# Kernel tuning notes

Measured on AMD Instinct MI355X. Metric: run time of the kernel, lower is better.

## Reference

```python
import jax, jax.numpy as jnp
import numpy as np

B = 512       # batch
N = 64        # max_nodes
H = 256       # hidden_dim
LAT = 128     # latent_dim
HEADS = 4
HC = H // HEADS   # per-head channels (GATConv out_channels)
NF = 64       # node_features
L = 3         # num_dec_layers
R = 8         # lora_r
SCAL = 16.0 / R   # lora_alpha / r
NB = 4        # num_bond_types
SLOPE = 0.2   # GATConv leaky_relu negative slope


def setup_inputs() -> dict:
    key = jax.random.key(0)
    ks = jax.random.split(key, 21)
    f = lambda k, shape, s=0.05: jax.random.normal(k, shape, dtype=jnp.float32) * s
    Din = H + LAT  # GAT input dim = hidden + latent (concat)
    return {
        "z": jax.random.normal(ks[0], (B, LAT), dtype=jnp.float32),
        # z_to_nodes LoRALinear: latent -> hidden*max_nodes
        "z2n_w": f(ks[1], (H * N, LAT)), "z2n_b": f(ks[2], (H * N,)),
        "z2n_A": f(ks[3], (R, LAT)), "z2n_B": f(ks[4], (H * N, R)),
        # GATConv stacks (same Din every layer): lin weight, att_src, att_dst, bias
        "gat_W": f(ks[5], (L, HEADS * HC, Din)),
        "gat_asrc": f(ks[6], (L, HEADS, HC)),
        "gat_adst": f(ks[7], (L, HEADS, HC)),
        "gat_bias": f(ks[8], (L, H)),
        # node predictor LoRALinear: hidden -> node_features
        "node_w": f(ks[9], (NF, H)), "node_b": f(ks[10], (NF,)),
        "node_A": f(ks[11], (R, H)), "node_B": f(ks[12], (NF, R)),
        # adj predictor LoRALinear: 2*hidden -> 1
        "adj_w": f(ks[13], (1, 2 * H)), "adj_b": f(ks[14], (1,)),
        "adj_A": f(ks[15], (R, 2 * H)), "adj_B": f(ks[16], (1, R)),
        # bond type predictor LoRALinear: 2*hidden -> 4
        "bond_w": f(ks[17], (NB, 2 * H)), "bond_b": f(ks[18], (NB,)),
        "bond_A": f(ks[19], (R, 2 * H)), "bond_B": f(ks[20], (NB, R)),
    }


def _lora_w(W, A, Bm):
    # effective weight of LoRALinear (eval mode, dropout off): W + (alpha/r) * B @ A
    return W + SCAL * (Bm @ A)


def _forward(z, z2n_w, z2n_b, z2n_A, z2n_B, gat_W, gat_asrc, gat_adst, gat_bias,
             node_w, node_b, node_A, node_B, adj_w, adj_b, adj_A, adj_B,
             bond_w, bond_b, bond_A, bond_B):
    # z_to_nodes: LoRA linear + ReLU -> [B, N, H]
    x = jax.nn.relu(z @ _lora_w(z2n_w, z2n_A, z2n_B).T + z2n_b).reshape(B, N, H)
    z_bc = jnp.broadcast_to(z[:, None, :], (B, N, LAT))
    # Fully-connected graph (off-diagonal edges) + GATConv default self loops
    # => dense softmax attention over all N source nodes per target, per graph.
    for l in range(L):
        xc = jnp.concatenate([x, z_bc], axis=-1)                      # [B,N,H+LAT]
        Wr = gat_W[l].reshape(HEADS, HC, H + LAT)
        h = jnp.einsum('bnd,hcd->bnhc', xc, Wr)                        # [B,N,heads,HC]
        e_src = jnp.einsum('bnhc,hc->bnh', h, gat_asrc[l])             # source term
        e_dst = jnp.einsum('bnhc,hc->bnh', h, gat_adst[l])             # target term
        e = e_dst[:, :, None, :] + e_src[:, None, :, :]                # [B,i,j,heads]
        e = jnp.where(e > 0, e, SLOPE * e)                             # leaky_relu
        alpha = jax.nn.softmax(e, axis=2)                              # over sources j
        out = jnp.einsum('bijh,bjhc->bihc', alpha, h).reshape(B, N, H) + gat_bias[l]
        x = jax.nn.relu(out)
    # node reconstruction
    recon_nodes = x @ _lora_w(node_w, node_A, node_B).T + node_b       # [B,N,NF]
    # pairwise predictors: Linear(concat[h_i,h_j]) = W1 h_i + W2 h_j + b
    iu = jnp.triu(jnp.ones((N, N), dtype=bool), 1)
    Wa = _lora_w(adj_w, adj_A, adj_B)                                  # [1,2H]
    s1 = x @ Wa[:, :H].T                                               # [B,N,1]
    s2 = x @ Wa[:, H:].T
    Am = s1 + jnp.swapaxes(s2, 1, 2) + adj_b[0]                        # Am[i,j]=s1[i]+s2[j]
    adj_logits = jnp.where(iu, Am, jnp.where(iu.T, jnp.swapaxes(Am, 1, 2), 0.0))
    Wb = _lora_w(bond_w, bond_A, bond_B)                               # [NB,2H]
    t1 = x @ Wb[:, :H].T                                               # [B,N,NB]
    t2 = x @ Wb[:, H:].T
    Bm = t1[:, :, None, :] + t2[:, None, :, :] + bond_b                # [B,N,N,NB]
    bond_logits = jnp.where(iu[:, :, None], Bm,
                            jnp.where(iu.T[:, :, None], jnp.swapaxes(Bm, 1, 2), 0.0))
    return recon_nodes, adj_logits, bond_logits


def reference(z, z2n_w, z2n_b, z2n_A, z2n_B, gat_W, gat_asrc, gat_adst, gat_bias,
              node_w, node_b, node_A, node_B, adj_w, adj_b, adj_A, adj_B,
              bond_w, bond_b, bond_A, bond_B):
    return _forward(z, z2n_w, z2n_b, z2n_A, z2n_B, gat_W, gat_asrc, gat_adst, gat_bias,
                    node_w, node_b, node_A, node_B, adj_w, adj_b, adj_A, adj_B,
                    bond_w, bond_b, bond_A, bond_B)
```

## Files before the change

kernel.cpp:

```cpp
#include <hip/hip_runtime.h>


typedef float float4v __attribute__((ext_vector_type(4)));
typedef short short8v __attribute__((ext_vector_type(8)));
typedef uint  uint4v  __attribute__((ext_vector_type(4)));

struct alignas(8) us4 { ushort x, y, z, w; };

#define ZA_OFF 0UL
#define HZ_OFF 4096UL
#define EZ_OFF 397312UL
#define XBF_U   819200UL
#define ZBF_U   9207808UL
#define GWBF_U  9273344UL
#define WZBF_U  9568256UL
#define PW_U    11665408UL
#define WST_U   11759616UL

__device__ inline ushort f2bf(float f) {
    uint u = __float_as_uint(f);
    uint r = (u + 0x7FFFu + ((u >> 16) & 1u)) >> 16;
    return (ushort)r;
}
__device__ inline float bf2f(ushort u) { return __uint_as_float(((uint)u) << 16); }

__device__ inline uint cvtpk(float a, float b) {
    uint r;
    asm("v_cvt_pk_bf16_f32 %0, %1, %2" : "=v"(r) : "v"(a), "v"(b));
    return r;
}

__device__ inline int xidx(int r, int cu) {
    int ch = cu >> 3;
    return r * 256 + (((ch ^ (r & 7))) << 3) + (cu & 7);
}

struct P3 { short8v b0, b1, b2; };
__device__ inline P3 loadP3(const ushort* pw, int lo, int hi, int kk) {
    P3 f;
    f.b0 = *(const short8v*)(pw + (size_t)(      lo)*256 + kk*32 + hi*8);
    f.b1 = *(const short8v*)(pw + (size_t)(16  + lo)*256 + kk*32 + hi*8);
    f.b2 = *(const short8v*)(pw + (size_t)(32  + lo)*256 + kk*32 + hi*8);
    return f;
}
struct P2 { short8v b3, b4; };
__device__ inline P2 loadP2(const ushort* pw, int lo, int hi, int kk) {
    P2 f;
    f.b3 = *(const short8v*)(pw + (size_t)(48 + lo)*256 + kk*32 + hi*8);
    f.b4 = *(const short8v*)(pw + (size_t)(64 + lo)*256 + kk*32 + hi*8);
    return f;
}

__device__ inline void gll(const ushort* src, ushort* dst) {
    __builtin_amdgcn_global_load_lds(
        (const __attribute__((address_space(1))) void*)src,
        (__attribute__((address_space(3))) void*)dst, 16, 0, 0);
}

__device__ inline void stageW(ushort* dstHead, const ushort* srcHead, int c0h, int ln) {
    if (c0h == 0) {
        gll(srcHead +        ln*8, dstHead);
        gll(srcHead +  512 + ln*8, dstHead + 512);
        gll(srcHead + 2048 + ln*8, dstHead + 2048);
    } else {
        gll(srcHead + 1024 + ln*8, dstHead + 1024);
        gll(srcHead + 1536 + ln*8, dstHead + 1536);
    }
}

__global__ __launch_bounds__(256) void k_setup(
    const float* __restrict__ z, const float* __restrict__ z2nA,
    const float* __restrict__ nodeW, const float* __restrict__ nodeA, const float* __restrict__ nodeB,
    const float* __restrict__ adjW, const float* __restrict__ adjA, const float* __restrict__ adjB,
    const float* __restrict__ bondW, const float* __restrict__ bondA, const float* __restrict__ bondB,
    const float* __restrict__ gatW, const float* __restrict__ z2nw,
    const float* __restrict__ asrcp, const float* __restrict__ adstp,
    float* __restrict__ wsf)
{
    ushort* wsu = (ushort*)wsf;
    int gid = blockIdx.x * 256 + threadIdx.x;
    if (gid < 4096) {
        int b = gid >> 3, r = gid & 7;
        const float* zp = z + (size_t)b * 128;
        const float* ap = z2nA + (size_t)r * 128;
        float s = 0.f;
        #pragma unroll 8
        for (int k = 0; k < 128; ++k) s += zp[k] * ap[k];
        wsf[ZA_OFF + gid] = s;
    } else if (gid < 24576) {
        int idx = gid - 4096;
        int r = idx >> 8, c = idx & 255;
        float v = 0.f;
        if (r < 64) {
            float s = 0.f;
            #pragma unroll
            for (int k = 0; k < 8; ++k) s += nodeB[r*8+k] * nodeA[k*256+c];
            v = nodeW[r*256+c] + 2.0f * s;
        } else if (r < 66) {
            int off = (r - 64) * 256 + c;
            float s = 0.f;
            #pragma unroll
            for (int k = 0; k < 8; ++k) s += adjB[k] * adjA[k*512+off];
            v = adjW[off] + 2.0f * s;
        } else if (r < 70) {
            int q = r - 66;
            float s = 0.f;
            #pragma unroll
            for (int k = 0; k < 8; ++k) s += bondB[q*8+k] * bondA[k*512+c];
            v = bondW[q*512+c] + 2.0f * s;
        } else if (r < 74) {
            int q = r - 70;
            float s = 0.f;
            #pragma unroll
            for (int k = 0; k < 8; ++k) s += bondB[q*8+k] * bondA[k*512+256+c];
            v = bondW[q*512+256+c] + 2.0f * s;
        }
        wsu[PW_U + idx] = f2bf(v);
    } else if (gid < 55296) {
        int idx = gid - 24576;
        int lkk = idx / 1280;
        int rem = idx - lkk * 1280;
        int head = rem / 320;
        int rem2 = rem - head * 320;
        int frag = rem2 >> 6;
        int ln = rem2 & 63;
        int lo = ln & 15, hi = ln >> 4;
        int l = lkk >> 3, kk = lkk & 7;
        ushort* dst = wsu + WST_U + (size_t)idx * 8;
        if (frag < 4) {
            const float* srcw = gatW + ((size_t)(l*256 + head*64 + frag*16 + lo))*384 + kk*32 + hi*8;
            #pragma unroll
            for (int j = 0; j < 8; ++j) dst[j] = f2bf(srcw[j]);
        } else {
            float s[8] = {0.f,0.f,0.f,0.f,0.f,0.f,0.f,0.f};
            if (lo < 2) {
                const float* av = (lo == 0 ? asrcp : adstp) + l*256 + head*64;
                const float* wp = gatW + ((size_t)(l*256 + head*64))*384 + kk*32 + hi*8;
                for (int hc = 0; hc < 64; ++hc) {
                    float a = av[hc];
                    const float* wr = wp + (size_t)hc * 384;
                    #pragma unroll
                    for (int j = 0; j < 8; ++j) s[j] += wr[j] * a;
                }
            }
            #pragma unroll
            for (int j = 0; j < 8; ++j) dst[j] = f2bf(s[j]);
        }
    } else {
        int cid = gid - 55296;
        const float* src; ushort* dst; int idx;
        if (cid < 16384)        { src = z;     dst = wsu + ZBF_U;  idx = cid; }
        else if (cid < 90112)   { src = gatW;  dst = wsu + GWBF_U; idx = cid - 16384; }
        else if (cid < 614400)  { src = z2nw;  dst = wsu + WZBF_U; idx = cid - 90112; }
        else return;
        float4 v = ((const float4*)src)[idx];
        us4 o; o.x = f2bf(v.x); o.y = f2bf(v.y); o.z = f2bf(v.z); o.w = f2bf(v.w);
        ((us4*)dst)[idx] = o;
    }
}

__global__ __launch_bounds__(256) void k_z2n(
    const float* __restrict__ bias, const float* __restrict__ lB,
    const float* __restrict__ asrcp, const float* __restrict__ adstp,
    float* __restrict__ wsf)
{
    ushort* wsu = (ushort*)wsf;
    int t = threadIdx.x;
    int w = t >> 6, ln = t & 63, lo = ln & 15, hi = ln >> 4;

    if (blockIdx.x >= 512) {
        int bid2 = blockIdx.x - 512;
        int l = bid2 >> 3, bg = bid2 & 7;
        const ushort* wz = wsu + GWBF_U + (size_t)l * 98304;
        const ushort* zb = wsu + ZBF_U + (size_t)bg * 64 * 128;
        float4v acc[4][4];
        #pragma unroll
        for (int m = 0; m < 4; ++m)
            #pragma unroll
            for (int n = 0; n < 4; ++n) acc[m][n] = (float4v)(0.f);
        #pragma unroll
        for (int kk = 0; kk < 4; ++kk) {
            short8v a[4], bq[4];
            #pragma unroll
            for (int m = 0; m < 4; ++m)
                a[m] = *(const short8v*)(wz + (size_t)(w*64 + m*16 + lo)*384 + 256 + kk*32 + hi*8);
            #pragma unroll
            for (int n = 0; n < 4; ++n)
                bq[n] = *(const short8v*)(zb + (size_t)(n*16 + lo)*128 + kk*32 + hi*8);
            #pragma unroll
            for (int m = 0; m < 4; ++m)
                #pragma unroll
                for (int n = 0; n < 4; ++n)
                    acc[m][n] = __builtin_amdgcn_mfma_f32_16x16x32_bf16(a[m], bq[n], acc[m][n], 0, 0, 0);
        }
        float* hzp = wsf + HZ_OFF + (size_t)l * 131072;
        #pragma unroll
        for (int m = 0; m < 4; ++m)
            #pragma unroll
            for (int n = 0; n < 4; ++n)
                #pragma unroll
                for (int q = 0; q < 4; ++q)
                    hzp[(size_t)(bg*64 + n*16 + lo)*256 + w*64 + m*16 + hi*4 + q] = acc[m][n][q];
        float as_[4][4], ad_[4][4];
        #pragma unroll
        for (int m = 0; m < 4; ++m)
            #pragma unroll
            for (int q = 0; q < 4; ++q) {
                as_[m][q] = asrcp[l*256 + w*64 + m*16 + hi*4 + q];
                ad_[m][q] = adstp[l*256 + w*64 + m*16 + hi*4 + q];
            }
        #pragma unroll
        for (int n = 0; n < 4; ++n) {
            float ss = 0.f, dd = 0.f;
            #pragma unroll
            for (int m = 0; m < 4; ++m)
                #pragma unroll
                for (int q = 0; q < 4; ++q) {
                    ss += acc[m][n][q] * as_[m][q];
                    dd += acc[m][n][q] * ad_[m][q];
                }
            ss += __shfl_xor(ss, 16); ss += __shfl_xor(ss, 32);
            dd += __shfl_xor(dd, 16); dd += __shfl_xor(dd, 32);
            if (hi == 0) {
                int b = bg*64 + n*16 + lo;
                wsf[EZ_OFF + (size_t)(l*2 + 0)*2048 + (size_t)b*4 + w] = ss;
                wsf[EZ_OFF + (size_t)(l*2 + 1)*2048 + (size_t)b*4 + w] = dd;
            }
        }
        return;
    }

    int bm = blockIdx.x >> 6, bn = blockIdx.x & 63;
    int brow0 = bm * 64;
    int o0 = bn * 256 + w * 64;
    const ushort* wz = wsu + WZBF_U;
    const ushort* zb = wsu + ZBF_U;
    float4v acc[4][4];
    #pragma unroll
    for (int m = 0; m < 4; ++m)
        #pragma unroll
        for (int n = 0; n < 4; ++n) acc[m][n] = (float4v)(0.f);
    #pragma unroll
    for (int kk = 0; kk < 4; ++kk) {
        short8v a[4], bq[4];
        #pragma unroll
        for (int m = 0; m < 4; ++m)
            a[m] = *(const short8v*)(wz + (size_t)(o0 + m*16 + lo)*128 + kk*32 + hi*8);
        #pragma unroll
        for (int n = 0; n < 4; ++n)
            bq[n] = *(const short8v*)(zb + (size_t)(brow0 + n*16 + lo)*128 + kk*32 + hi*8);
        #pragma unroll
        for (int m = 0; m < 4; ++m)
            #pragma unroll
            for (int n = 0; n < 4; ++n)
                acc[m][n] = __builtin_amdgcn_mfma_f32_16x16x32_bf16(a[m], bq[n], acc[m][n], 0, 0, 0);
    }
    const float* zA = wsf + ZA_OFF;
    float4 za0[4], za1[4];
    #pragma unroll
    for (int n = 0; n < 4; ++n) {
        int brow = brow0 + n*16 + lo;
        za0[n] = *(const float4*)&zA[brow*8];
        za1[n] = *(const float4*)&zA[brow*8 + 4];
    }
    #pragma unroll
    for (int m = 0; m < 4; ++m) {
        float lor[4][4]; float bs[4];
        #pragma unroll
        for (int q = 0; q < 4; ++q) {
            int o = o0 + m*16 + hi*4 + q;
            float4 b20 = *(const float4*)&lB[(size_t)o*8];
            float4 b21 = *(const float4*)&lB[(size_t)o*8 + 4];
            bs[q] = bias[o];
            #pragma unroll
            for (int n = 0; n < 4; ++n)
                lor[n][q] = za0[n].x*b20.x + za0[n].y*b20.y + za0[n].z*b20.z + za0[n].w*b20.w
                          + za1[n].x*b21.x + za1[n].y*b21.y + za1[n].z*b21.z + za1[n].w*b21.w;
        }
        #pragma unroll
        for (int n = 0; n < 4; ++n) {
            int brow = brow0 + n*16 + lo;
            float v0 = acc[m][n][0] + 2.f*lor[n][0] + bs[0]; v0 = v0 > 0.f ? v0 : 0.f;
            float v1 = acc[m][n][1] + 2.f*lor[n][1] + bs[1]; v1 = v1 > 0.f ? v1 : 0.f;
            float v2 = acc[m][n][2] + 2.f*lor[n][2] + bs[2]; v2 = v2 > 0.f ? v2 : 0.f;
            float v3 = acc[m][n][3] + 2.f*lor[n][3] + bs[3]; v3 = v3 > 0.f ? v3 : 0.f;
            us4 pk; pk.x = f2bf(v0); pk.y = f2bf(v1); pk.z = f2bf(v2); pk.w = f2bf(v3);
            *(us4*)(wsu + XBF_U + (size_t)brow*16384 + o0 + m*16 + hi*4) = pk;
        }
    }
}

__global__ __launch_bounds__(512, 4) void k_fused(
    const float* __restrict__ gbias,
    const float* __restrict__ nodeb, const float* __restrict__ adjb,
    const float* __restrict__ bondb,
    float* __restrict__ wsf, float* __restrict__ out)
{
    extern __shared__ ushort dyn[];
    ushort* Rr   = dyn;
    ushort* bbuf = dyn + 17408;
    float*  scr  = (float*)(dyn + 17408 + 20480);
    ushort* wsu = (ushort*)wsf;
    int t = threadIdx.x;
    int w = t >> 6, ln = t & 63, lo = ln & 15, hi = ln >> 4;
    int head = w & 3, m0 = (w >> 2) * 32;
    int headH = w >> 1, c0h = w & 1;
    int b = blockIdx.x;
    const ushort* xb = wsu + XBF_U + (size_t)b * 16384;

    #pragma unroll
    for (int i = 0; i < 4; ++i) {
        int flat = i*512 + t;
        int r = flat >> 5, ch = flat & 31;
        short8v v = *(const short8v*)(xb + (size_t)r*256 + ch*8);
        *(short8v*)&Rr[r*256 + ((ch ^ (r & 7)) << 3)] = v;
    }
    __syncthreads();

    float* es = scr;
    float* ed = scr + 256;

    {
        const ushort* wst0 = wsu + WST_U;
        stageW(bbuf +         headH*2560, wst0 +         headH*2560, c0h, ln);
        stageW(bbuf + 10240 + headH*2560, wst0 + 10240 + headH*2560, c0h, ln);
    }

    for (int l = 0; l < 3; ++l) {
        const ushort* wst  = wsu + WST_U + (size_t)l * 81920;
        const ushort* wstN = wsu + WST_U + (size_t)(l + 1) * 81920;
        const float*  hzp = wsf + HZ_OFF + (size_t)l*131072 + (size_t)b*256 + headH*64;

        float hzA = hzp[(c0h*2    )*16 + lo];
        float hzB = hzp[(c0h*2 + 1)*16 + lo];
        float ezs = wsf[EZ_OFF + (size_t)(l*2 + 0)*2048 + (size_t)b*4 + headH];
        float ezd = wsf[EZ_OFF + (size_t)(l*2 + 1)*2048 + (size_t)b*4 + headH];

        float4v acc[2][4], accE[4];
        float eInit = (lo == 0) ? ezs : (lo == 1 ? ezd : 0.f);
        #pragma unroll
        for (int m = 0; m < 4; ++m) {
            acc[0][m] = (float4v)(hzA);
            acc[1][m] = (float4v)(hzB);
            accE[m]   = (float4v)(eInit);
        }

        #pragma unroll
        for (int kk = 0; kk < 8; ++kk) {
            if (kk == 7 && l == 2) {
                asm volatile("s_waitcnt vmcnt(0)" ::: "memory");
            } else if (c0h == 0) {
                asm volatile("s_waitcnt vmcnt(3)" ::: "memory");
            } else {
                asm volatile("s_waitcnt vmcnt(2)" ::: "memory");
            }
            const ushort* bb = bbuf + (kk&1)*10240 + headH*2560;
            short8v bq0 = *(const short8v*)(bb + (c0h*2    )*512 + ln*8);
            short8v bq1 = *(const short8v*)(bb + (c0h*2 + 1)*512 + ln*8);
            short8v bsd = {};
            if (c0h == 0) bsd = *(const short8v*)(bb + 2048 + ln*8);
            short8v a0 = *(const short8v*)&Rr[xidx(     lo, kk*32 + hi*8)];
            short8v a1 = *(const short8v*)&Rr[xidx(16 + lo, kk*32 + hi*8)];
            short8v a2 = *(const short8v*)&Rr[xidx(32 + lo, kk*32 + hi*8)];
            short8v a3 = *(const short8v*)&Rr[xidx(48 + lo, kk*32 + hi*8)];
            if (kk < 6) {
                asm volatile("s_waitcnt lgkmcnt(0)" ::: "memory");
                stageW(bbuf + (kk&1)*10240 + headH*2560,
                       wst + (size_t)(kk+2)*10240 + headH*2560, c0h, ln);
            } else if (l < 2) {
                asm volatile("s_waitcnt lgkmcnt(0)" ::: "memory");
                stageW(bbuf + (kk&1)*10240 + headH*2560,
                       wstN + (size_t)(kk-6)*10240 + headH*2560, c0h, ln);
            }
            __builtin_amdgcn_s_setprio(1);
            acc[0][0] = __builtin_amdgcn_mfma_f32_16x16x32_bf16(a0, bq0, acc[0][0], 0, 0, 0);
            acc[0][1] = __builtin_amdgcn_mfma_f32_16x16x32_bf16(a1, bq0, acc[0][1], 0, 0, 0);
            acc[0][2] = __builtin_amdgcn_mfma_f32_16x16x32_bf16(a2, bq0, acc[0][2], 0, 0, 0);
            acc[0][3] = __builtin_amdgcn_mfma_f32_16x16x32_bf16(a3, bq0, acc[0][3], 0, 0, 0);
            acc[1][0] = __builtin_amdgcn_mfma_f32_16x16x32_bf16(a0, bq1, acc[1][0], 0, 0, 0);
            acc[1][1] = __builtin_amdgcn_mfma_f32_16x16x32_bf16(a1, bq1, acc[1][1], 0, 0, 0);
            acc[1][2] = __builtin_amdgcn_mfma_f32_16x16x32_bf16(a2, bq1, acc[1][2], 0, 0, 0);
            acc[1][3] = __builtin_amdgcn_mfma_f32_16x16x32_bf16(a3, bq1, acc[1][3], 0, 0, 0);
            if (c0h == 0) {
                accE[0] = __builtin_amdgcn_mfma_f32_16x16x32_bf16(a0, bsd, accE[0], 0, 0, 0);
                accE[1] = __builtin_amdgcn_mfma_f32_16x16x32_bf16(a1, bsd, accE[1], 0, 0, 0);
                accE[2] = __builtin_amdgcn_mfma_f32_16x16x32_bf16(a2, bsd, accE[2], 0, 0, 0);
                accE[3] = __builtin_amdgcn_mfma_f32_16x16x32_bf16(a3, bsd, accE[3], 0, 0, 0);
            }
            __builtin_amdgcn_s_setprio(0);
        }

        if (c0h == 0) {
            if (lo == 0) {
                #pragma unroll
                for (int m = 0; m < 4; ++m)
                    *(float4*)&es[headH*64 + m*16 + hi*4] =
                        make_float4(accE[m][0], accE[m][1], accE[m][2], accE[m][3]);
            } else if (lo == 1) {
                #pragma unroll
                for (int m = 0; m < 4; ++m)
                    *(float4*)&ed[headH*64 + m*16 + hi*4] =
                        make_float4(accE[m][0], accE[m][1], accE[m][2], accE[m][3]);
            }
        }

        __syncthreads();

        #pragma unroll
        for (int cf = 0; cf < 2; ++cf)
            #pragma unroll
            for (int m = 0; m < 4; ++m) {
                uint2 pk;
                pk.x = cvtpk(acc[cf][m][0], acc[cf][m][1]);
                pk.y = cvtpk(acc[cf][m][2], acc[cf][m][3]);
                *(uint2*)&Rr[headH*4352 + ((c0h*2 + cf)*16 + lo)*68 + m*16 + hi*4] = pk;
            }

        __syncthreads();

        float4v acc2[4][2];
        #pragma unroll
        for (int m = 0; m < 4; ++m)
            #pragma unroll
            for (int n = 0; n < 2; ++n) acc2[m][n] = (float4v)(0.f);
        float psum[2] = {0.f, 0.f};
        #pragma unroll
        for (int kk = 0; kk < 2; ++kk) {
            short8v hb[4];
            #pragma unroll
            for (int m = 0; m < 4; ++m)
                hb[m] = *(const short8v*)&Rr[head*4352 + (m*16 + lo)*68 + kk*32 + hi*8];
            float4 e0 = *(const float4*)&es[head*64 + kk*32 + hi*8];
            float4 e1 = *(const float4*)&es[head*64 + kk*32 + hi*8 + 4];
            float ej[8] = {e0.x, e0.y, e0.z, e0.w, e1.x, e1.y, e1.z, e1.w};
            #pragma unroll
            for (int n = 0; n < 2; ++n) {
                float edr = ed[head*64 + m0 + n*16 + lo];
                float pvv[8]; float pp = 0.f;
                #pragma unroll
                for (int jj = 0; jj < 8; ++jj) {
                    float e = edr + ej[jj];
                    e = fmaxf(e, 0.2f * e);
                    float p = __expf(e);
                    pp += p;
                    pvv[jj] = p;
                }
                uint4v au;
                au.x = cvtpk(pvv[0], pvv[1]); au.y = cvtpk(pvv[2], pvv[3]);
                au.z = cvtpk(pvv[4], pvv[5]); au.w = cvtpk(pvv[6], pvv[7]);
                short8v af = __builtin_bit_cast(short8v, au);
                psum[n] += pp;
                __builtin_amdgcn_s_setprio(1);
                #pragma unroll
                for (int m = 0; m < 4; ++m)
                    acc2[m][n] = __builtin_amdgcn_mfma_f32_16x16x32_bf16(hb[m], af, acc2[m][n], 0, 0, 0);
                __builtin_amdgcn_s_setprio(0);
            }
        }
        float rs[2];
        #pragma unroll
        for (int n = 0; n < 2; ++n) {
            psum[n] += __shfl_xor(psum[n], 16);
            psum[n] += __shfl_xor(psum[n], 32);
            rs[n] = 1.0f / psum[n];
        }

        __syncthreads();

        #pragma unroll
        for (int m = 0; m < 4; ++m) {
            int c0 = head*64 + m*16 + hi*4;
            float b0f = gbias[l*256 + c0 + 0];
            float b1f = gbias[l*256 + c0 + 1];
            float b2f = gbias[l*256 + c0 + 2];
            float b3f = gbias[l*256 + c0 + 3];
            #pragma unroll
            for (int n = 0; n < 2; ++n) {
                int r = m0 + n*16 + lo;
                float v0 = acc2[m][n][0]*rs[n] + b0f; v0 = v0 > 0.f ? v0 : 0.f;
                float v1 = acc2[m][n][1]*rs[n] + b1f; v1 = v1 > 0.f ? v1 : 0.f;
                float v2 = acc2[m][n][2]*rs[n] + b2f; v2 = v2 > 0.f ? v2 : 0.f;
                float v3 = acc2[m][n][3]*rs[n] + b3f; v3 = v3 > 0.f ? v3 : 0.f;
                uint2 pk; pk.x = cvtpk(v0, v1); pk.y = cvtpk(v2, v3);
                *(uint2*)&Rr[xidx(r, c0)] = pk;
            }
        }

        __syncthreads();
    }

    const ushort* pw = wsu + PW_U;
    int pq = w & 3, pn = w >> 2;
    if (pn == 0) {
        float4v p0 = (float4v)(0.f), p1 = (float4v)(0.f), p2 = (float4v)(0.f);
        P3 fA = loadP3(pw, lo, hi, 0);
        #pragma unroll
        for (int ii = 0; ii < 4; ++ii) {
            P3 fB = loadP3(pw, lo, hi, 2*ii + 1);
            {
                int kk = 2*ii;
                short8v a = *(const short8v*)&Rr[xidx(pq*16 + lo, kk*32 + hi*8)];
                p0 = __builtin_amdgcn_mfma_f32_16x16x32_bf16(a, fA.b0, p0, 0, 0, 0);
                p1 = __builtin_amdgcn_mfma_f32_16x16x32_bf16(a, fA.b1, p1, 0, 0, 0);
                p2 = __builtin_amdgcn_mfma_f32_16x16x32_bf16(a, fA.b2, p2, 0, 0, 0);
            }
            if (ii < 3) fA = loadP3(pw, lo, hi, 2*ii + 2);
            {
                int kk = 2*ii + 1;
                short8v a = *(const short8v*)&Rr[xidx(pq*16 + lo, kk*32 + hi*8)];
                p0 = __builtin_amdgcn_mfma_f32_16x16x32_bf16(a, fB.b0, p0, 0, 0, 0);
                p1 = __builtin_amdgcn_mfma_f32_16x16x32_bf16(a, fB.b1, p1, 0, 0, 0);
                p2 = __builtin_amdgcn_mfma_f32_16x16x32_bf16(a, fB.b2, p2, 0, 0, 0);
            }
        }
        __syncthreads();
        float* Rf = (float*)Rr;
        #pragma unroll
        for (int qq = 0; qq < 4; ++qq) {
            int nd = pq*16 + hi*4 + qq;
            Rf[nd*68 + lo]      = p0[qq];
            Rf[nd*68 + 16 + lo] = p1[qq];
            Rf[nd*68 + 32 + lo] = p2[qq];
        }
    } else {
        float4v p3 = (float4v)(0.f), paux = (float4v)(0.f);
        P2 fA = loadP2(pw, lo, hi, 0);
        #pragma unroll
        for (int ii = 0; ii < 4; ++ii) {
            P2 fB = loadP2(pw, lo, hi, 2*ii + 1);
            {
                int kk = 2*ii;
                short8v a = *(const short8v*)&Rr[xidx(pq*16 + lo, kk*32 + hi*8)];
                p3   = __builtin_amdgcn_mfma_f32_16x16x32_bf16(a, fA.b3, p3, 0, 0, 0);
                paux = __builtin_amdgcn_mfma_f32_16x16x32_bf16(a, fA.b4, paux, 0, 0, 0);
            }
            if (ii < 3) fA = loadP2(pw, lo, hi, 2*ii + 2);
            {
                int kk = 2*ii + 1;
                short8v a = *(const short8v*)&Rr[xidx(pq*16 + lo, kk*32 + hi*8)];
                p3   = __builtin_amdgcn_mfma_f32_16x16x32_bf16(a, fB.b3, p3, 0, 0, 0);
                paux = __builtin_amdgcn_mfma_f32_16x16x32_bf16(a, fB.b4, paux, 0, 0, 0);
            }
        }
        __syncthreads();
        float* Rf = (float*)Rr;
        #pragma unroll
        for (int qq = 0; qq < 4; ++qq) {
            int nd = pq*16 + hi*4 + qq;
            Rf[nd*68 + 48 + lo] = p3[qq];
            float v = paux[qq];
            if (lo == 0)      scr[nd] = v;
            else if (lo == 1) scr[64 + nd] = v;
            else if (lo < 6)  scr[128 + nd*5 + (lo-2)] = v;
            else if (lo < 10) scr[448 + nd*5 + (lo-6)] = v;
        }
    }
    __syncthreads();

    {
        const float* Rf = (const float*)Rr;
        #pragma unroll
        for (int it = 0; it < 2; ++it) {
            int idx = it*512 + t;
            int nd = idx >> 4, f0 = (idx & 15) * 4;
            float4 v = *(const float4*)&Rf[nd*68 + f0];
            float4 bv = *(const float4*)&nodeb[f0];
            v.x += bv.x; v.y += bv.y; v.z += bv.z; v.w += bv.w;
            *(float4*)&out[(size_t)b*4096 + (size_t)idx*4] = v;
        }
    }

    float ab = adjb[0];
    #pragma unroll
    for (int it = 0; it < 2; ++it) {
        int idx = it*512 + t;
        int flat = idx * 4;
        int i = flat >> 6, j0 = flat & 63;
        float4 v; float* vp = (float*)&v;
        #pragma unroll
        for (int uu = 0; uu < 4; ++uu) {
            int j = j0 + uu;
            float val;
            if (i == j)      val = 0.f;
            else if (i < j)  val = scr[i] + scr[64 + j] + ab;
            else             val = scr[j] + scr[64 + i] + ab;
            vp[uu] = val;
        }
        *(float4*)&out[2097152UL + (size_t)b*4096 + flat] = v;
    }

    float4 bb2 = *(const float4*)bondb;
    #pragma unroll
    for (int it = 0; it < 8; ++it) {
        int fl4 = it*512 + t;
        int i = fl4 >> 6, j = fl4 & 63;
        float4 v;
        if (i == j) { v.x = v.y = v.z = v.w = 0.f; }
        else {
            int a2 = i < j ? i : j, c2 = i < j ? j : i;
            v.x = scr[128 + a2*5 + 0] + scr[448 + c2*5 + 0] + bb2.x;
            v.y = scr[128 + a2*5 + 1] + scr[448 + c2*5 + 1] + bb2.y;
            v.z = scr[128 + a2*5 + 2] + scr[448 + c2*5 + 2] + bb2.z;
            v.w = scr[128 + a2*5 + 3] + scr[448 + c2*5 + 3] + bb2.w;
        }
        *(float4*)&out[4194304UL + (size_t)b*16384 + (size_t)fl4*4] = v;
    }
}

extern "C" void kernel_launch(void* const* d_in, const int* in_sizes, int n_in,
                              void* d_out, int out_size, void* d_ws, size_t ws_size,
                              hipStream_t stream)
{
    const float* z     = (const float*)d_in[0];
    const float* z2nw  = (const float*)d_in[1];
    const float* z2nb  = (const float*)d_in[2];
    const float* z2nA  = (const float*)d_in[3];
    const float* z2nB  = (const float*)d_in[4];
    const float* gatW  = (const float*)d_in[5];
    const float* asrc  = (const float*)d_in[6];
    const float* adst  = (const float*)d_in[7];
    const float* gbias = (const float*)d_in[8];
    const float* nodew = (const float*)d_in[9];
    const float* nodeb = (const float*)d_in[10];
    const float* nodeA = (const float*)d_in[11];
    const float* nodeB = (const float*)d_in[12];
    const float* adjw  = (const float*)d_in[13];
    const float* adjb  = (const float*)d_in[14];
    const float* adjA  = (const float*)d_in[15];
    const float* adjB  = (const float*)d_in[16];
    const float* bondw = (const float*)d_in[17];
    const float* bondb = (const float*)d_in[18];
    const float* bondA = (const float*)d_in[19];
    const float* bondB = (const float*)d_in[20];
    float* ws  = (float*)d_ws;
    float* out = (float*)d_out;

    k_setup<<<2616, 256, 0, stream>>>(z, z2nA, nodew, nodeA, nodeB,
                                      adjw, adjA, adjB, bondw, bondA, bondB,
                                      gatW, z2nw, asrc, adst, ws);
    k_z2n<<<536, 256, 0, stream>>>(z2nb, z2nB, asrc, adst, ws);
    k_fused<<<512, 512, 78848, stream>>>(gbias, nodeb, adjb, bondb, ws, out);
}
```

Before: 86.50 us.

## Pre-swizzle z2n weights into MFMA fragment order and stage via LDS DMA

The setup kernel now writes the bf16 z_to_nodes weight in a fragment-ordered layout, so each wave's A-operand tile sits in contiguous memory. The z2n GEMM copies these tiles into a double-buffered shared-memory array with global_load_lds and reads MFMA fragments from LDS, instead of strided per-row global loads. The goal is fully coalesced weight traffic and overlap of the next K-slice load with the current MFMAs. In exchange every block reserves 32KB of LDS, which may reduce occupancy, and a barrier is added per K step.

```diff
diff --git a/kernel.cpp b/kernel.cpp
--- a/kernel.cpp
+++ b/kernel.cpp
@@ -13,7 +13,7 @@
 #define XBF_U   819200UL
 #define ZBF_U   9207808UL
 #define GWBF_U  9273344UL
-#define WZBF_U  9568256UL
+#define WZST_U  9568256UL
 #define PW_U    11665408UL
 #define WST_U   11759616UL
 
@@ -66,6 +66,12 @@
         gll(srcHead + 1024 + ln*8, dstHead + 1024);
         gll(srcHead + 1536 + ln*8, dstHead + 1536);
     }
+}
+
+__device__ inline void stageZ(ushort* dst, const ushort* src, int ln) {
+    #pragma unroll
+    for (int c = 0; c < 4; ++c)
+        gll(src + c*512 + ln*8, dst + c*512);
 }
 
 __global__ __launch_bounds__(256) void k_setup(
@@ -148,14 +154,27 @@
         }
     } else {
         int cid = gid - 55296;
-        const float* src; ushort* dst; int idx;
-        if (cid < 16384)        { src = z;     dst = wsu + ZBF_U;  idx = cid; }
-        else if (cid < 90112)   { src = gatW;  dst = wsu + GWBF_U; idx = cid - 16384; }
-        else if (cid < 614400)  { src = z2nw;  dst = wsu + WZBF_U; idx = cid - 90112; }
-        else return;
-        float4 v = ((const float4*)src)[idx];
-        us4 o; o.x = f2bf(v.x); o.y = f2bf(v.y); o.z = f2bf(v.z); o.w = f2bf(v.w);
-        ((us4*)dst)[idx] = o;
+        if (cid < 16384) {
+            float4 v = ((const float4*)z)[cid];
+            us4 o; o.x = f2bf(v.x); o.y = f2bf(v.y); o.z = f2bf(v.z); o.w = f2bf(v.w);
+            ((us4*)(wsu + ZBF_U))[cid] = o;
+        } else if (cid < 90112) {
+            int idx = cid - 16384;
+            float4 v = ((const float4*)gatW)[idx];
+            us4 o; o.x = f2bf(v.x); o.y = f2bf(v.y); o.z = f2bf(v.z); o.w = f2bf(v.w);
+            ((us4*)(wsu + GWBF_U))[idx] = o;
+        } else if (cid < 614400) {
+            int idx = cid - 90112;
+            int o = idx >> 5;
+            int k = (idx & 31) * 4;
+            float4 v = ((const float4*)z2nw)[idx];
+            int bn = o >> 8, wv = (o >> 6) & 3, frag = (o >> 4) & 3, lo2 = o & 15;
+            int kk2 = k >> 5, hi2 = (k >> 3) & 3, j = k & 7;
+            int ln2 = hi2*16 + lo2;
+            size_t off = ((((size_t)(bn*4 + kk2)*4 + wv)*4 + frag)*64 + ln2)*8 + j;
+            us4 oo; oo.x = f2bf(v.x); oo.y = f2bf(v.y); oo.z = f2bf(v.z); oo.w = f2bf(v.w);
+            *(us4*)(wsu + WZST_U + off) = oo;
+        }
     }
 }
 
@@ -164,6 +183,7 @@
     const float* __restrict__ asrcp, const float* __restrict__ adstp,
     float* __restrict__ wsf)
 {
+    __shared__ ushort wbuf[16384];
     ushort* wsu = (ushort*)wsf;
     int t = threadIdx.x;
     int w = t >> 6, ln = t & 63, lo = ln & 15, hi = ln >> 4;
@@ -233,19 +253,26 @@
     int bm = blockIdx.x >> 6, bn = blockIdx.x & 63;
     int brow0 = bm * 64;
     int o0 = bn * 256 + w * 64;
-    const ushort* wz = wsu + WZBF_U;
+    const ushort* wst = wsu + WZST_U + (size_t)bn * 32768;
     const ushort* zb = wsu + ZBF_U;
     float4v acc[4][4];
     #pragma unroll
     for (int m = 0; m < 4; ++m)
         #pragma unroll
         for (int n = 0; n < 4; ++n) acc[m][n] = (float4v)(0.f);
+
+    stageZ(wbuf + w*2048, wst + w*2048, ln);
+
     #pragma unroll
     for (int kk = 0; kk < 4; ++kk) {
+        __syncthreads();
+        if (kk < 3)
+            stageZ(wbuf + ((kk+1)&1)*8192 + w*2048,
+                   wst + (size_t)(kk+1)*8192 + w*2048, ln);
         short8v a[4], bq[4];
         #pragma unroll
         for (int m = 0; m < 4; ++m)
-            a[m] = *(const short8v*)(wz + (size_t)(o0 + m*16 + lo)*128 + kk*32 + hi*8);
+            a[m] = *(const short8v*)&wbuf[(kk&1)*8192 + w*2048 + m*512 + ln*8];
         #pragma unroll
         for (int n = 0; n < 4; ++n)
             bq[n] = *(const short8v*)(zb + (size_t)(brow0 + n*16 + lo)*128 + kk*32 + hi*8);
```

Result: faster. 84.77 us (-2.0%).
